# Performance work log

Measured on AMD Instinct MI355X. Metric: run time of the kernel, lower is better.

## Reference

```python
import jax, jax.numpy as jnp
import numpy as np

MARGIN = 0.3


def setup_inputs() -> dict:
    key = jax.random.key(0)
    k1, k2 = jax.random.split(key)
    inputs = jax.random.normal(k1, (8192, 256), dtype=jnp.float32)
    targets = jax.random.randint(k2, (8192,), 0, 512, dtype=jnp.int64)
    return {"inputs": inputs, "targets": targets}


def reference(inputs, targets):
    # L2-normalize features (normalize_feature=True default)
    x = inputs / (jnp.linalg.norm(inputs, axis=-1, keepdims=True) + 1e-12)
    n = x.shape[0]
    # pairwise euclidean distance [n, n]
    sq = jnp.sum(x * x, axis=1)
    dist = sq[:, None] + sq[None, :] - 2.0 * (x @ x.T)
    dist = jnp.sqrt(jnp.clip(dist, 1e-12, None))
    # positive / negative masks
    same = targets[:, None] == targets[None, :]
    eye = jnp.eye(n, dtype=bool)
    is_same = same & ~eye          # positives, diagonal excluded
    is_diff = ~same                # negatives
    neg_inf = jnp.float32(-jnp.inf)
    pos_inf = jnp.float32(jnp.inf)
    # hard positive: max over positives per row (fallback 0.0 if none)
    dist_ap = jnp.max(jnp.where(is_same, dist, neg_inf), axis=1)
    dist_ap = jnp.where(jnp.any(is_same, axis=1), dist_ap, 0.0)
    # hard negative: min over negatives per row (fallback margin+1 if none)
    dist_an = jnp.min(jnp.where(is_diff, dist, pos_inf), axis=1)
    dist_an = jnp.where(jnp.any(is_diff, axis=1), dist_an, MARGIN + 1.0)
    # MarginRankingLoss with y=1: mean(max(0, -(an - ap) + margin))
    loss = jnp.mean(jnp.maximum(0.0, dist_ap - dist_an + MARGIN))
    return loss
```

## Files before the change

### kernel.cpp

```cpp
#include <hip/hip_runtime.h>
#include <hip/hip_bf16.h>

#define NROWS  8192
#define DIM    256
#define MARGIN 0.3f

using bf16x8 = __attribute__((ext_vector_type(8))) short;
using f32x4  = __attribute__((ext_vector_type(4))) float;

__device__ inline ushort f2bf(float f) {
    __hip_bfloat16 h = __float2bfloat16(f);
    return *reinterpret_cast<ushort*>(&h);
}
__device__ inline float bf2f(ushort u) {
    return __uint_as_float(((unsigned)u) << 16);
}
__device__ inline unsigned f2ord(float f) {
    unsigned b = __float_as_uint(f);
    return (b & 0x80000000u) ? ~b : (b | 0x80000000u);
}
__device__ inline float ord2f(unsigned u) {
    return __uint_as_float((u & 0x80000000u) ? (u & 0x7FFFFFFFu) : ~u);
}
__device__ inline void ld16_g2l(const void* g, void* l) {
    __builtin_amdgcn_global_load_lds(
        (const __attribute__((address_space(1))) unsigned int*)g,
        (__attribute__((address_space(3))) unsigned int*)l, 16, 0, 0);
}

#define XBS_OFF 0u
#define SQS_OFF 4194304u
#define PMX_OFF 4259840u
#define NMN_OFF 4292608u
#define ACC_OFF 4327424u
#define TIK_OFF 4327432u

__global__ __launch_bounds__(256) void norm_kernel(
    const float* __restrict__ in, ushort* __restrict__ xbs,
    float* __restrict__ sqs, unsigned* __restrict__ pmax,
    unsigned* __restrict__ nmin, double* __restrict__ accd,
    unsigned* __restrict__ ticket)
{
    int row  = blockIdx.x * 4 + (threadIdx.x >> 6);
    int lane = threadIdx.x & 63;
    if (blockIdx.x == 0 && threadIdx.x == 0) { *accd = 0.0; *ticket = 0u; }
    float4 v = ((const float4*)(in + (size_t)row * DIM))[lane];
    float ss = v.x * v.x + v.y * v.y + v.z * v.z + v.w * v.w;
#pragma unroll
    for (int m = 1; m < 64; m <<= 1) ss += __shfl_xor(ss, m, 64);
    float inv = 1.0f / (sqrtf(ss) + 1e-12f);

    ushort4 st;
    st.x = f2bf(v.x * inv); st.y = f2bf(v.y * inv);
    st.z = f2bf(v.z * inv); st.w = f2bf(v.w * inv);

    ((ushort4*)(xbs + (size_t)row * DIM))[lane] = st;

    float a0 = bf2f(st.x), a1 = bf2f(st.y), a2 = bf2f(st.z), a3 = bf2f(st.w);
    float s2 = a0 * a0 + a1 * a1 + a2 * a2 + a3 * a3;
#pragma unroll
    for (int m = 1; m < 64; m <<= 1) s2 += __shfl_xor(s2, m, 64);
    if (lane == 0) {
        sqs[row]  = s2;
        pmax[row] = 0x007FFFFFu;
        nmin[row] = 0xFF800000u;
    }
}

__global__ __launch_bounds__(256, 2) void gram_kernel(
    const ushort* __restrict__ xbs, const float* __restrict__ sqs,
    const int* __restrict__ tgt, unsigned* __restrict__ pmax,
    unsigned* __restrict__ nmin)
{
    __shared__ struct {
        char  buf[3][16384];
        float sqc[512];
        int   tgc[512];
        int   tga[256];
    } sm;

    const int wave = threadIdx.x >> 6;
    const int lane = threadIdx.x & 63;
    const int l15  = lane & 15;
    const int quad = lane >> 4;
    const int mbase = blockIdx.x * 256 + wave * 64;
    const int nbase = blockIdx.y * 512;

    {
        int c = threadIdx.x * 2;
        sm.sqc[c]     = sqs[nbase + c];
        sm.sqc[c + 1] = sqs[nbase + c + 1];
        sm.tgc[c]     = tgt[nbase + c];
        sm.tgc[c + 1] = tgt[nbase + c + 1];
        sm.tga[threadIdx.x] = tgt[blockIdx.x * 256 + threadIdx.x];
    }

    bf16x8 afrag[4][8];
#pragma unroll
    for (int a = 0; a < 4; ++a) {
        const ushort* arow = xbs + (size_t)(mbase + a * 16 + l15) * DIM + quad * 8;
#pragma unroll
        for (int kk = 0; kk < 8; ++kk)
            afrag[a][kk] = *(const bf16x8*)(arow + kk * 32);
    }

    const int colh = lane >> 5, c31 = lane & 31;
    int offs[4];
#pragma unroll
    for (int j = 0; j < 4; ++j)
        offs[j] = colh * 512 + ((c31 ^ ((2 * j + colh) & 7)) << 4);

    const char* xbs_b = (const char*)xbs;

    {
        const char* g0 = xbs_b + (size_t)nbase * 512;
        const char* g1 = xbs_b + (size_t)(nbase + 32) * 512;
#pragma unroll
        for (int j = 0; j < 4; ++j) {
            int i = wave * 4 + j;
            ld16_g2l(g0 + i * 1024 + offs[j], sm.buf[0] + i * 1024);
            ld16_g2l(g1 + i * 1024 + offs[j], sm.buf[1] + i * 1024);
        }
    }
    __syncthreads();

    float pm[16], nm[16];
#pragma unroll
    for (int j = 0; j < 16; ++j) { pm[j] = -__builtin_inff(); nm[j] = __builtin_inff(); }

#define COMPUTE_STAGE(bufc_, s_) do {                                        \
        _Pragma("unroll")                                                    \
        for (int u = 0; u < 2; ++u) {                                        \
            const int t16 = (s_) * 32 + u * 16;                              \
            bf16x8 bfrag[8];                                                 \
            _Pragma("unroll")                                                \
            for (int kk = 0; kk < 8; ++kk)                                   \
                bfrag[kk] = *(const bf16x8*)((bufc_) + u * 8192 + l15 * 512 + \
                                             (((quad + 4 * kk) ^ (l15 & 7)) << 4)); \
            f32x4 acc4[4];                                                   \
            _Pragma("unroll")                                                \
            for (int a = 0; a < 4; ++a) {                                    \
                f32x4 acc = {0.f, 0.f, 0.f, 0.f};                            \
                _Pragma("unroll")                                            \
                for (int kk = 0; kk < 8; ++kk)                               \
                    acc = __builtin_amdgcn_mfma_f32_16x16x32_bf16(           \
                              afrag[a][kk], bfrag[kk], acc, 0, 0, 0);        \
                acc4[a] = acc;                                               \
            }                                                                \
            const float sqc = sm.sqc[t16 + l15];                             \
            const int   tc  = sm.tgc[t16 + l15];                             \
            _Pragma("unroll")                                                \
            for (int a = 0; a < 4; ++a)                                      \
                _Pragma("unroll")                                            \
                for (int i = 0; i < 4; ++i) {                                \
                    const float v = fmaf(acc4[a][i], -2.0f, sqc);            \
                    const bool same = (sm.tga[wave * 64 + a * 16 + quad * 4 + i] == tc); \
                    pm[a * 4 + i] = fmaxf(pm[a * 4 + i], same ? v : -__builtin_inff()); \
                    nm[a * 4 + i] = fminf(nm[a * 4 + i], same ? __builtin_inff() : v);  \
                }                                                            \
        }                                                                    \
    } while (0)

    char* pA = sm.buf[0];
    char* pB = sm.buf[1];
    char* pC = sm.buf[2];

#pragma unroll 1
    for (int s = 0; s < 15; ++s) {
        asm volatile("s_waitcnt vmcnt(4)" ::: "memory");
        __builtin_amdgcn_sched_barrier(0);
        __builtin_amdgcn_s_barrier();
        __builtin_amdgcn_sched_barrier(0);
        if (s < 14) {
            const char* gbase = xbs_b + (size_t)(nbase + (s + 2) * 32) * 512;
#pragma unroll
            for (int j = 0; j < 4; ++j) {
                int i = wave * 4 + j;
                ld16_g2l(gbase + i * 1024 + offs[j], pC + i * 1024);
            }
        }
        COMPUTE_STAGE(pA, s);
        char* t = pA; pA = pB; pB = pC; pC = t;
    }
    asm volatile("s_waitcnt vmcnt(0)" ::: "memory");
    __builtin_amdgcn_sched_barrier(0);
    __builtin_amdgcn_s_barrier();
    __builtin_amdgcn_sched_barrier(0);
    COMPUTE_STAGE(pA, 15);
#undef COMPUTE_STAGE

#pragma unroll
    for (int m = 1; m < 16; m <<= 1) {
#pragma unroll
        for (int j = 0; j < 16; ++j) {
            pm[j] = fmaxf(pm[j], __shfl_xor(pm[j], m, 64));
            nm[j] = fminf(nm[j], __shfl_xor(nm[j], m, 64));
        }
    }
    if (l15 == 0) {
#pragma unroll
        for (int a = 0; a < 4; ++a)
#pragma unroll
            for (int i = 0; i < 4; ++i) {
                int r = mbase + a * 16 + quad * 4 + i;
                atomicMax(&pmax[r], f2ord(pm[a * 4 + i]));
                atomicMin(&nmin[r], f2ord(nm[a * 4 + i]));
            }
    }
}

__global__ __launch_bounds__(256) void finalize_kernel(
    const unsigned* __restrict__ pmax, const unsigned* __restrict__ nmin,
    const float* __restrict__ sqs, double* __restrict__ accd,
    unsigned* __restrict__ ticket, float* __restrict__ out)
{
    int r = blockIdx.x * 256 + threadIdx.x;
    float pe = ord2f(pmax[r]);
    float ne = ord2f(nmin[r]);
    float ap = sqrtf(fmaxf(sqs[r] + pe, 0.0f));
    float an = (ne > 1e30f) ? (MARGIN + 1.0f) : sqrtf(fmaxf(sqs[r] + ne, 0.0f));
    float h  = fmaxf(ap - an + MARGIN, 0.0f);
    double s = (double)h;
#pragma unroll
    for (int m = 1; m < 64; m <<= 1) s += __shfl_xor(s, m, 64);
    __shared__ double sh[4];
    if ((threadIdx.x & 63) == 0) sh[threadIdx.x >> 6] = s;
    __syncthreads();
    if (threadIdx.x == 0) {
        double b = sh[0] + sh[1] + sh[2] + sh[3];
        atomicAdd(accd, b);
        __threadfence();
        unsigned old = atomicAdd(ticket, 1u);
        if (old == gridDim.x - 1) {
            double total = atomicAdd(accd, 0.0);
            out[0] = (float)(total / (double)NROWS);
        }
    }
}

extern "C" void kernel_launch(void* const* d_in, const int* in_sizes, int n_in,
                              void* d_out, int out_size, void* d_ws, size_t ws_size,
                              hipStream_t stream) {
    const float* in  = (const float*)d_in[0];
    const int*   tgt = (const int*)d_in[1];
    float*       out = (float*)d_out;

    char* ws = (char*)d_ws;
    ushort*   xbs    = (ushort*)(ws + XBS_OFF);
    float*    sqs    = (float*)(ws + SQS_OFF);
    unsigned* pmax   = (unsigned*)(ws + PMX_OFF);
    unsigned* nmin   = (unsigned*)(ws + NMN_OFF);
    double*   accd   = (double*)(ws + ACC_OFF);
    unsigned* ticket = (unsigned*)(ws + TIK_OFF);

    norm_kernel<<<NROWS / 4, 256, 0, stream>>>(in, xbs, sqs, pmax, nmin, accd, ticket);
    gram_kernel<<<dim3(32, 16), 256, 0, stream>>>(xbs, sqs, tgt, pmax, nmin);
    finalize_kernel<<<32, 256, 0, stream>>>(pmax, nmin, sqs, accd, ticket, out);
}
```

Baseline: 108.9 us.

## Split each stage into ping-pong half-K phases with barriers and MFMA priority

Restructures the main loop so each 32-column stage runs as four sub-phases. Each sub-phase issues LDS reads for half the K fragments, interleaves part of the next global-to-LDS prefetch, synchronises waves with s_barrier, and runs the MFMAs at raised s_setprio. The epilogue for the first 16-column tile is moved so it overlaps the reads for the second tile. The aim is to spread memory issue across phases and keep MFMA units busy across waves, in the style of ping-pong scheduling. In exchange it adds several extra barriers per stage and lgkmcnt(0) waits, which could cost more in stalls than the overlap gains.

```diff
diff --git a/kernel.cpp b/kernel.cpp
--- a/kernel.cpp
+++ b/kernel.cpp
@@ -128,66 +128,122 @@
 #pragma unroll
     for (int j = 0; j < 16; ++j) { pm[j] = -__builtin_inff(); nm[j] = __builtin_inff(); }
 
-#define COMPUTE_STAGE(bufc_, s_) do {                                        \
+#define DSREAD_HALF(dst_, base_, u_, h_)                                     \
+    _Pragma("unroll")                                                        \
+    for (int kk = 0; kk < 4; ++kk)                                           \
+        dst_[kk] = *(const bf16x8*)((base_) + (u_) * 8192 + l15 * 512 +      \
+                    (((quad + 4 * (kk + 4 * (h_))) ^ (l15 & 7)) << 4));
+
+#define MFMA_HALF(bf_, h_)                                                   \
+    _Pragma("unroll")                                                        \
+    for (int kk = 0; kk < 4; ++kk)                                           \
         _Pragma("unroll")                                                    \
-        for (int u = 0; u < 2; ++u) {                                        \
-            const int t16 = (s_) * 32 + u * 16;                              \
-            bf16x8 bfrag[8];                                                 \
+        for (int a = 0; a < 4; ++a)                                          \
+            acc4[a] = __builtin_amdgcn_mfma_f32_16x16x32_bf16(               \
+                          afrag[a][kk + 4 * (h_)], bf_[kk], acc4[a], 0, 0, 0);
+
+#define EPILOG(t16_)                                                         \
+    {                                                                        \
+        const float sqc_ = sm.sqc[(t16_) + l15];                             \
+        const int   tc_  = sm.tgc[(t16_) + l15];                             \
+        _Pragma("unroll")                                                    \
+        for (int a = 0; a < 4; ++a)                                          \
             _Pragma("unroll")                                                \
-            for (int kk = 0; kk < 8; ++kk)                                   \
-                bfrag[kk] = *(const bf16x8*)((bufc_) + u * 8192 + l15 * 512 + \
-                                             (((quad + 4 * kk) ^ (l15 & 7)) << 4)); \
-            f32x4 acc4[4];                                                   \
-            _Pragma("unroll")                                                \
-            for (int a = 0; a < 4; ++a) {                                    \
-                f32x4 acc = {0.f, 0.f, 0.f, 0.f};                            \
-                _Pragma("unroll")                                            \
-                for (int kk = 0; kk < 8; ++kk)                               \
-                    acc = __builtin_amdgcn_mfma_f32_16x16x32_bf16(           \
-                              afrag[a][kk], bfrag[kk], acc, 0, 0, 0);        \
-                acc4[a] = acc;                                               \
+            for (int i = 0; i < 4; ++i) {                                    \
+                const float v_ = fmaf(acc4[a][i], -2.0f, sqc_);              \
+                const bool same_ = (sm.tga[wave * 64 + a * 16 + quad * 4 + i] == tc_); \
+                pm[a * 4 + i] = fmaxf(pm[a * 4 + i], same_ ? v_ : -__builtin_inff()); \
+                nm[a * 4 + i] = fminf(nm[a * 4 + i], same_ ? __builtin_inff() : v_);  \
             }                                                                \
-            const float sqc = sm.sqc[t16 + l15];                             \
-            const int   tc  = sm.tgc[t16 + l15];                             \
-            _Pragma("unroll")                                                \
-            for (int a = 0; a < 4; ++a)                                      \
-                _Pragma("unroll")                                            \
-                for (int i = 0; i < 4; ++i) {                                \
-                    const float v = fmaf(acc4[a][i], -2.0f, sqc);            \
-                    const bool same = (sm.tga[wave * 64 + a * 16 + quad * 4 + i] == tc); \
-                    pm[a * 4 + i] = fmaxf(pm[a * 4 + i], same ? v : -__builtin_inff()); \
-                    nm[a * 4 + i] = fminf(nm[a * 4 + i], same ? __builtin_inff() : v);  \
-                }                                                            \
+    }
+
+#define ISSUE2(j0_)                                                          \
+    if (s < 14) {                                                            \
+        _Pragma("unroll")                                                    \
+        for (int j = (j0_); j < (j0_) + 2; ++j) {                            \
+            int i = wave * 4 + j;                                            \
+            ld16_g2l(gnext + i * 1024 + offs[j], pC + i * 1024);             \
         }                                                                    \
-    } while (0)
+    }
+
+#define LGKM0_SB  do { asm volatile("s_waitcnt lgkmcnt(0)" ::: "memory");    \
+                       __builtin_amdgcn_sched_barrier(0); } while (0)
 
     char* pA = sm.buf[0];
     char* pB = sm.buf[1];
     char* pC = sm.buf[2];
 
 #pragma unroll 1
-    for (int s = 0; s < 15; ++s) {
-        asm volatile("s_waitcnt vmcnt(4)" ::: "memory");
-        __builtin_amdgcn_sched_barrier(0);
-        __builtin_amdgcn_s_barrier();
-        __builtin_amdgcn_sched_barrier(0);
-        if (s < 14) {
-            const char* gbase = xbs_b + (size_t)(nbase + (s + 2) * 32) * 512;
-#pragma unroll
-            for (int j = 0; j < 4; ++j) {
-                int i = wave * 4 + j;
-                ld16_g2l(gbase + i * 1024 + offs[j], pC + i * 1024);
+    for (int s = 0; s < 16; ++s) {
+        const char* gnext = xbs_b + (size_t)(nbase + (s + 2) * 32) * 512;
+        f32x4 acc4[4];
+#pragma unroll
+        for (int a = 0; a < 4; ++a) acc4[a] = (f32x4){0.f, 0.f, 0.f, 0.f};
+
+        {
+            bf16x8 bfh[4];
+            DSREAD_HALF(bfh, pA, 0, 0);
+            ISSUE2(0);
+            __builtin_amdgcn_s_barrier();
+            LGKM0_SB;
+            __builtin_amdgcn_s_setprio(1);
+            MFMA_HALF(bfh, 0);
+            __builtin_amdgcn_s_setprio(0);
+            __builtin_amdgcn_sched_barrier(0);
+            __builtin_amdgcn_s_barrier();
+        }
+        {
+            bf16x8 bfh[4];
+            DSREAD_HALF(bfh, pA, 0, 1);
+            ISSUE2(2);
+            __builtin_amdgcn_s_barrier();
+            LGKM0_SB;
+            __builtin_amdgcn_s_setprio(1);
+            MFMA_HALF(bfh, 1);
+            __builtin_amdgcn_s_setprio(0);
+            __builtin_amdgcn_sched_barrier(0);
+            __builtin_amdgcn_s_barrier();
+        }
+        {
+            bf16x8 bfh[4];
+            DSREAD_HALF(bfh, pA, 1, 0);
+            EPILOG(s * 32);
+#pragma unroll
+            for (int a = 0; a < 4; ++a) acc4[a] = (f32x4){0.f, 0.f, 0.f, 0.f};
+            __builtin_amdgcn_s_barrier();
+            LGKM0_SB;
+            __builtin_amdgcn_s_setprio(1);
+            MFMA_HALF(bfh, 0);
+            __builtin_amdgcn_s_setprio(0);
+            __builtin_amdgcn_sched_barrier(0);
+            __builtin_amdgcn_s_barrier();
+        }
+        {
+            bf16x8 bfh[4];
+            DSREAD_HALF(bfh, pA, 1, 1);
+            __builtin_amdgcn_s_barrier();
+            LGKM0_SB;
+            __builtin_amdgcn_s_setprio(1);
+            MFMA_HALF(bfh, 1);
+            __builtin_amdgcn_s_setprio(0);
+            __builtin_amdgcn_sched_barrier(0);
+            if (s < 14) {
+                asm volatile("s_waitcnt vmcnt(4)" ::: "memory");
+            } else if (s == 14) {
+                asm volatile("s_waitcnt vmcnt(0)" ::: "memory");
             }
-        }
-        COMPUTE_STAGE(pA, s);
+            __builtin_amdgcn_sched_barrier(0);
+            __builtin_amdgcn_s_barrier();
+        }
+        EPILOG(s * 32 + 16);
+
         char* t = pA; pA = pB; pB = pC; pC = t;
     }
-    asm volatile("s_waitcnt vmcnt(0)" ::: "memory");
-    __builtin_amdgcn_sched_barrier(0);
-    __builtin_amdgcn_s_barrier();
-    __builtin_amdgcn_sched_barrier(0);
-    COMPUTE_STAGE(pA, 15);
-#undef COMPUTE_STAGE
+#undef DSREAD_HALF
+#undef MFMA_HALF
+#undef EPILOG
+#undef ISSUE2
+#undef LGKM0_SB
 
 #pragma unroll
     for (int m = 1; m < 16; m <<= 1) {
```

After: 109.9 us. About the same (+0.9%).
